# Performance work log

Measured on AMD Instinct MI355X. Metric: run time of the kernel, lower is better.

The kernel has to match this reference:

```python
import jax, jax.numpy as jnp
import numpy as np

KSIZE, STRIDE, H, W = 7, 4, 128, 128
NH = (H - KSIZE) // STRIDE + 1  # 31
L = NH * NH                     # 961 patches


def conv2d(x, w, b=None, stride=1):
    y = jax.lax.conv_general_dilated(x, w, (stride, stride), 'VALID',
                                     dimension_numbers=('NCHW', 'OIHW', 'NCHW'))
    if b is not None:
        y = y + b[None, :, None, None]
    return y


def refpad(x):
    return jnp.pad(x, ((0, 0), (0, 0), (1, 1), (1, 1)), mode='reflect')


def unfold(x, k, s):
    # torch.nn.Unfold equivalent, returned as (B, C, k, k, L)
    B, C, Hh, Ww = x.shape
    nh = (Hh - k) // s + 1
    nw = (Ww - k) // s + 1
    hi = (jnp.arange(nh) * s)[:, None] + jnp.arange(k)  # (nh, k)
    wi = (jnp.arange(nw) * s)[:, None] + jnp.arange(k)  # (nw, k)
    p = x[:, :, hi]            # (B, C, nh, k, W)
    p = p[:, :, :, :, wi]      # (B, C, nh, k, nw, k)
    p = p.transpose(0, 1, 3, 5, 2, 4).reshape(B, C, k, k, nh * nw)
    return p


def fold(patches, Hh, Ww, k, s):
    # patches: (B, nh, nw, C, k, k); overlap-add like torch.nn.functional.fold
    B, nh, nw, C = patches.shape[0], patches.shape[1], patches.shape[2], patches.shape[3]
    hi = (jnp.arange(nh) * s)[:, None] + jnp.arange(k)  # (nh, k)
    wi = (jnp.arange(nw) * s)[:, None] + jnp.arange(k)  # (nw, k)
    H_idx = hi[:, None, :, None]  # (nh, 1, k, 1)
    W_idx = wi[None, :, None, :]  # (1, nw, 1, k)
    vals = patches.transpose(0, 3, 1, 2, 4, 5)  # (B, C, nh, nw, k, k)
    out = jnp.zeros((B, C, Hh, Ww), patches.dtype)
    return out.at[:, :, H_idx, W_idx].add(vals)


def setup_inputs() -> dict:
    key = jax.random.key(0)
    ks = jax.random.split(key, 16)
    Cin, Ci = 32, 16            # in_channels, inter_channels
    F_in = KSIZE * KSIZE * Ci   # 784
    F_out = F_in // 4           # 196
    s = 0.05
    d = {
        'x':       jax.random.normal(ks[0], (8, Cin, H, W), jnp.float32),
        'g_w':     jax.random.normal(ks[1], (Ci, Cin, 3, 3), jnp.float32) * s,
        'g_b':     jax.random.normal(ks[2], (Ci,), jnp.float32) * s,
        'w_w':     jax.random.normal(ks[3], (Ci, Cin, 3, 3), jnp.float32) * s,
        'w_b':     jax.random.normal(ks[4], (Ci,), jnp.float32) * s,
        'theta_w': jax.random.normal(ks[5], (Cin, Ci, 1, 1), jnp.float32) * s,
        'theta_b': jax.random.normal(ks[6], (Cin,), jnp.float32) * s,
        'fc1_w':   jax.random.normal(ks[7], (F_out, F_in), jnp.float32) * s,
        'fc1_b':   jax.random.normal(ks[8], (F_out,), jnp.float32) * s,
        'mconv_w': jax.random.normal(ks[9], (L, L), jnp.float32) * s,
        'mconv_b': jax.random.normal(ks[10], (L,), jnp.float32) * s,
        'mfc_w':   jax.random.normal(ks[11], (L, L), jnp.float32) * s,
        'mfc_b':   jax.random.normal(ks[12], (L,), jnp.float32) * s,
        'c1_w':    jax.random.normal(ks[13], (Cin // 2, Cin, 3, 3), jnp.float32) * s,
        'c2_w':    jax.random.normal(ks[14], (Cin, Cin // 2, 1, 1), jnp.float32) * s,
    }
    return d


def reference(x, g_w, g_b, w_w, w_b, theta_w, theta_b, fc1_w, fc1_b,
              mconv_w, mconv_b, mfc_w, mfc_b, c1_w, c2_w):
    residual = x
    x1 = conv2d(refpad(x), g_w, g_b)        # (B, Ci, H, W)
    x2 = conv2d(refpad(x), w_w, w_b)        # (B, Ci, H, W)
    x3 = conv2d(x1, theta_w, theta_b)       # (B, Cin, H, W)
    B = x.shape[0]
    Cin = x.shape[1]

    p6 = unfold(x1, KSIZE, STRIDE).transpose(0, 4, 1, 2, 3).reshape(B, L, -1)   # (B,L,Ci*49)
    p4 = unfold(x2, KSIZE, STRIDE).transpose(0, 4, 1, 2, 3).reshape(B, L, -1)   # (B,L,Ci*49)
    p62 = unfold(x3, KSIZE, STRIDE).transpose(0, 4, 1, 2, 3).reshape(B, L, -1)  # (B,L,Cin*49)

    wf = p4 @ fc1_w.T + fc1_b   # (B, L, F)
    xf = p6 @ fc1_w.T + fc1_b   # (B, L, F)
    A = jnp.einsum('blf,bmf->blm', wf, xf)  # (B, L, L)

    # Ti1 (Conv1d k=1 over patch dim) + Ti2 (Linear over patch dim, transposed)
    Ti = jnp.einsum('nc,bcm->bnm', mconv_w + mfc_w, A) + (mconv_b + mfc_b)[None, :, None]
    mask = jax.nn.sigmoid(Ti)
    mask_b = (mask != 0.0).astype(A.dtype)

    scale = wf.shape[-1] ** -0.5
    Am = jax.nn.softmax(A * mask * scale, axis=-1) * mask_b  # (B, L, L)

    y = jnp.einsum('blm,bmf->blf', Am, p62)  # (B, L, Cin*49)
    y = y.reshape(B, NH, NH, Cin, KSIZE, KSIZE)
    out = fold(y, H, W, KSIZE, STRIDE)       # (B, Cin, H, W)

    # BasicBlock: conv3x3(reflect) -> lrelu -> conv1x1 -> lrelu
    o = jax.nn.leaky_relu(conv2d(refpad(out), c1_w), 0.2)
    o = jax.nn.leaky_relu(conv2d(o, c2_w), 0.2)
    out = residual + o
    return Am, out
```

## Files before the change

### kernel.cpp

```cpp
#include <hip/hip_runtime.h>
#include <math.h>

namespace {
constexpr int Bn   = 8;
constexpr int CIN  = 32;
constexpr int CI   = 16;
constexpr int Lp   = 961;
constexpr int FIN  = 784;
constexpr int FOUT = 196;
constexpr int F62  = 1568;

constexpr int FCP  = 224;
constexpr long long FCB = 961LL * FCP;
constexpr int KP   = 992;
constexpr long long WFTB = 196LL * KP;
constexpr long long AMBB = 961LL * KP;
constexpr long long PBTB = 1568LL * KP;
constexpr long long AB   = 961LL * 961;
constexpr int YLD  = 964;
constexpr long long YB = 1568LL * YLD;
}

typedef __attribute__((ext_vector_type(8))) short short8x;
typedef __attribute__((ext_vector_type(4))) float floatx4;
typedef __attribute__((ext_vector_type(4))) unsigned short ushort4x;

static __device__ __forceinline__ unsigned short f2bf(float x) {
    unsigned int u = __builtin_bit_cast(unsigned int, x);
    u += 0x7fffu + ((u >> 16) & 1u);
    return (unsigned short)(u >> 16);
}
static __device__ __forceinline__ float bf2f(unsigned short h) {
    return __builtin_bit_cast(float, ((unsigned int)h) << 16);
}

__global__ __launch_bounds__(256)
void prep_k(const float* __restrict__ g_w, const float* __restrict__ w_w,
            const float* __restrict__ c1_w,
            float* __restrict__ wT1, float* __restrict__ wT2,
            float* __restrict__ wTc,
            const float* __restrict__ mconv_w, const float* __restrict__ mfc_w,
            unsigned short* __restrict__ Mwh, unsigned short* __restrict__ Mwl,
            const float* __restrict__ mconv_b, const float* __restrict__ mfc_b,
            float* __restrict__ Mb,
            const float* __restrict__ fc1w,
            unsigned short* __restrict__ Wh, unsigned short* __restrict__ Wl,
            unsigned short* __restrict__ wfTh, unsigned short* __restrict__ wfTl)
{
    int i = blockIdx.x * 256 + threadIdx.x;
    if (i < 13824) {
        int sel = i / 4608, r = i - sel * 4608;
        int tapidx = r >> 4, co = r & 15;
        const float* w = (sel == 0) ? g_w : (sel == 1) ? w_w : c1_w;
        float* t = (sel == 0) ? wT1 : (sel == 1) ? wT2 : wTc;
        t[r] = w[co * 288 + tapidx];
    } else if (i < 967136) {
        int k = i - 13824;
        int n = k / KP, c = k - n * KP;
        float v = (c < 961) ? (mconv_w[n * 961 + c] + mfc_w[n * 961 + c]) : 0.0f;
        unsigned short h = f2bf(v);
        Mwh[k] = h; Mwl[k] = f2bf(v - bf2f(h));
    } else if (i < 968097) {
        int k = i - 967136;
        Mb[k] = mconv_b[k] + mfc_b[k];
    } else if (i < 1172897) {
        int k = i - 968097;
        int n = k / 800, kk = k - n * 800;
        float v = (n < 196 && kk < 784) ? fc1w[n * 784 + kk] : 0.0f;
        unsigned short h = f2bf(v);
        Wh[k] = h; Wl[k] = f2bf(v - bf2f(h));
    } else if (i < 1223073) {
        int k = i - 1172897;
        int row = k >> 5, c = k & 31;
        long long pos = (long long)row * KP + 960 + c;
        wfTh[pos] = 0; wfTl[pos] = 0;
    }
}

template<bool DUAL, bool BIAS, bool LEAKY>
__global__ __launch_bounds__(256)
void conv3x3t_k(const float* __restrict__ x,
                const float* __restrict__ wT1, const float* __restrict__ b1,
                const float* __restrict__ wT2, const float* __restrict__ b2,
                float* __restrict__ o1, float* __restrict__ o2)
{
    __shared__ float Ls[10880];
    const int tid = threadIdx.x;
    const int t  = blockIdx.x;
    const int wt = t & 3, ht = (t >> 2) & 15, b = t >> 6;
    const int h0 = ht * 8, w0 = wt * 32;
    const float* xb = x + (size_t)b * CIN * 16384;

    for (int i = tid; i < 10880; i += 256) {
        int ci  = i / 340;
        int rem = i - ci * 340;
        int row = rem / 34;
        int col = rem - row * 34;
        int gh = h0 + row - 1; gh = (gh < 0) ? 1 : (gh > 127 ? 126 : gh);
        int gw = w0 + col - 1; gw = (gw < 0) ? 1 : (gw > 127 ? 126 : gw);
        Ls[i] = xb[ci * 16384 + gh * 128 + gw];
    }
    __syncthreads();

    const int px = tid & 31, py = tid >> 5;
    float acc1[16], acc2[16];
    #pragma unroll
    for (int co = 0; co < 16; ++co) {
        acc1[co] = BIAS ? b1[co] : 0.0f;
        acc2[co] = (DUAL && BIAS) ? b2[co] : 0.0f;
    }

    for (int ci = 0; ci < 32; ++ci) {
        const float* lp = &Ls[ci * 340 + py * 34 + px];
        float vv[9];
        #pragma unroll
        for (int r = 0; r < 3; ++r)
            #pragma unroll
            for (int c = 0; c < 3; ++c)
                vv[r * 3 + c] = lp[r * 34 + c];
        const float* wr1 = wT1 + ci * 144;
        const float* wr2 = DUAL ? (wT2 + ci * 144) : nullptr;
        #pragma unroll
        for (int tp = 0; tp < 9; ++tp) {
            float v = vv[tp];
            #pragma unroll
            for (int co = 0; co < 16; ++co) {
                acc1[co] += v * wr1[tp * 16 + co];
                if constexpr (DUAL) acc2[co] += v * wr2[tp * 16 + co];
            }
        }
    }

    const int h = h0 + py, w = w0 + px;
    size_t ob = (((size_t)b * 16) * 128 + h) * 128 + w;
    #pragma unroll
    for (int co = 0; co < 16; ++co) {
        float v = acc1[co];
        if constexpr (LEAKY) v = (v >= 0.0f) ? v : 0.2f * v;
        o1[ob + (size_t)co * 16384] = v;
        if constexpr (DUAL) o2[ob + (size_t)co * 16384] = acc2[co];
    }
}

template<bool BIAS, bool LEAKY, bool RESID>
__global__ __launch_bounds__(256)
void conv1x1p_k(const float* __restrict__ src, const float* __restrict__ wgt,
                const float* __restrict__ bias, const float* __restrict__ resid,
                float* __restrict__ out)
{
    int idx = blockIdx.x * 256 + threadIdx.x;
    int pix = idx & 16383;
    int b   = idx >> 14;
    const float* sb = src + (size_t)b * CI * 16384 + pix;
    float s[16];
    #pragma unroll
    for (int ci = 0; ci < CI; ++ci) s[ci] = sb[ci * 16384];
    size_t ob = (size_t)b * 32 * 16384 + pix;
    #pragma unroll
    for (int co = 0; co < 32; ++co) {
        const float* wrow = wgt + co * CI;
        float acc = BIAS ? bias[co] : 0.0f;
        #pragma unroll
        for (int ci = 0; ci < CI; ++ci) acc += wrow[ci] * s[ci];
        if constexpr (LEAKY) acc = (acc >= 0.0f) ? acc : 0.2f * acc;
        if constexpr (RESID) acc += resid[ob + (size_t)co * 16384];
        out[ob + (size_t)co * 16384] = acc;
    }
}

template<bool WRT>
__global__ __launch_bounds__(256)
void fcmfma_k(const float* __restrict__ xsrc,
              const unsigned short* __restrict__ Wh,
              const unsigned short* __restrict__ Wl,
              const float* __restrict__ bias,
              unsigned short* __restrict__ Dh, unsigned short* __restrict__ Dl,
              unsigned short* __restrict__ DTh, unsigned short* __restrict__ DTl)
{
    __shared__ unsigned short AsH[64*32], AsL[64*32], BsH[64*32], BsL[64*32];
    const int tid = threadIdx.x;
    const int tm0 = (blockIdx.x >> 2) * 64;
    const int tn0 = (blockIdx.x & 3) * 64;

    const int lr = tid >> 2;
    const int lc = tid & 3;
    const int gm = tm0 + lr;
    const bool mok = gm < 7688;
    int gbase = 0;
    if (mok) {
        int b = gm / 961, pi = gm - b * 961;
        int ih = pi / 31, iw = pi - ih * 31;
        gbase = b * 262144 + ih * 512 + iw * 4;
    }
    const int pc = ((lc ^ ((lr >> 1) & 3))) * 8;
    const unsigned short* Whr = Wh + (tn0 + lr) * 800;
    const unsigned short* Wlr = Wl + (tn0 + lr) * 800;

    const int lane = tid & 63, wv = tid >> 6;
    const int wm = (wv >> 1) * 32, wn = (wv & 1) * 32;
    const int fr = lane & 15, kq = lane >> 4;

    floatx4 acc[2][2];
    #pragma unroll
    for (int i = 0; i < 2; ++i)
        #pragma unroll
        for (int j = 0; j < 2; ++j)
            acc[i][j] = (floatx4){0.f, 0.f, 0.f, 0.f};

    float pv[8];
    short8x pwh, pwl;
    auto loadA = [&](int k0) {
        #pragma unroll
        for (int j = 0; j < 8; ++j) {
            int k = k0 + lc * 8 + j;
            float v = 0.0f;
            if (mok && k < 784) {
                int c  = k / 49, r = k - c * 49;
                int kh = r / 7,  kw = r - kh * 7;
                v = xsrc[gbase + c * 16384 + kh * 128 + kw];
            }
            pv[j] = v;
        }
    };
    auto loadW = [&](int k0) {
        pwh = *(const short8x*)(Whr + k0 + lc * 8);
        pwl = *(const short8x*)(Wlr + k0 + lc * 8);
    };

    loadA(0); loadW(0);
    for (int k0 = 0; k0 < 800; k0 += 32) {
        unsigned short hv[8], lv[8];
        #pragma unroll
        for (int j = 0; j < 8; ++j) {
            unsigned short h = f2bf(pv[j]);
            hv[j] = h; lv[j] = f2bf(pv[j] - bf2f(h));
        }
        *(short8x*)&AsH[lr * 32 + pc] = *(short8x*)hv;
        *(short8x*)&AsL[lr * 32 + pc] = *(short8x*)lv;
        *(short8x*)&BsH[lr * 32 + pc] = pwh;
        *(short8x*)&BsL[lr * 32 + pc] = pwl;
        __syncthreads();
        if (k0 + 32 < 800) { loadA(k0 + 32); loadW(k0 + 32); }
        short8x ah[2], al[2], bh[2], bl[2];
        #pragma unroll
        for (int i = 0; i < 2; ++i) {
            int mr = wm + i * 16 + fr;
            int off = mr * 32 + ((kq ^ ((mr >> 1) & 3)) * 8);
            ah[i] = *(const short8x*)&AsH[off];
            al[i] = *(const short8x*)&AsL[off];
        }
        #pragma unroll
        for (int j = 0; j < 2; ++j) {
            int nr = wn + j * 16 + fr;
            int off = nr * 32 + ((kq ^ ((nr >> 1) & 3)) * 8);
            bh[j] = *(const short8x*)&BsH[off];
            bl[j] = *(const short8x*)&BsL[off];
        }
        #pragma unroll
        for (int i = 0; i < 2; ++i)
            #pragma unroll
            for (int j = 0; j < 2; ++j) {
                acc[i][j] = __builtin_amdgcn_mfma_f32_16x16x32_bf16(ah[i], bh[j], acc[i][j], 0, 0, 0);
                acc[i][j] = __builtin_amdgcn_mfma_f32_16x16x32_bf16(ah[i], bl[j], acc[i][j], 0, 0, 0);
                acc[i][j] = __builtin_amdgcn_mfma_f32_16x16x32_bf16(al[i], bh[j], acc[i][j], 0, 0, 0);
            }
        __syncthreads();
    }

    #pragma unroll
    for (int j = 0; j < 2; ++j) {
        int n = tn0 + wn + j * 16 + fr;
        if (n >= FCP) continue;
        float bn = (n < 196) ? bias[n] : 0.0f;
        #pragma unroll
        for (int i = 0; i < 2; ++i) {
            #pragma unroll
            for (int r = 0; r < 4; ++r) {
                int l = tm0 + wm + i * 16 + kq * 4 + r;
                if (l >= 7688) continue;
                int b = l / 961, pi = l - b * 961;
                float v = (n < 196) ? (acc[i][j][r] + bn) : 0.0f;
                unsigned short h = f2bf(v);
                unsigned short lo = f2bf(v - bf2f(h));
                long long base = (long long)b * FCB + (long long)pi * FCP + n;
                Dh[base] = h;
                Dl[base] = lo;
                if constexpr (WRT) {
                    if (n < 196) {
                        long long tb = (long long)b * WFTB + (long long)n * KP + pi;
                        DTh[tb] = h;
                        DTl[tb] = lo;
                    }
                }
            }
        }
    }
}

__global__ __launch_bounds__(256)
void w2mfma_k(const unsigned short* __restrict__ Xhi,
              const unsigned short* __restrict__ Xlo,
              const unsigned short* __restrict__ Yhi,
              const unsigned short* __restrict__ Ylo,
              unsigned short* __restrict__ W2h,
              unsigned short* __restrict__ W2l)
{
    __shared__ unsigned short XsH[4096], XsL[4096], YsH[4096], YsL[4096];
    const int b   = blockIdx.x & 7;
    const int t   = blockIdx.x >> 3;
    const int tm0 = (t >> 1) * 128;
    const int tn0 = (t & 1) * 128;
    const unsigned short* Ybh = Yhi + (long long)b * WFTB;
    const unsigned short* Ybl = Ylo + (long long)b * WFTB;
    const int tid = threadIdx.x;

    const int sr  = tid >> 1;
    const int sc0 = (tid & 1) * 2;
    const bool xok = (tm0 + sr) < 961;
    const bool yok = (tn0 + sr) < 196;
    const unsigned short* Xrh = Xhi + (long long)(tm0 + sr) * KP;
    const unsigned short* Xrl = Xlo + (long long)(tm0 + sr) * KP;
    const unsigned short* Yrh = Ybh + (long long)(tn0 + sr) * KP;
    const unsigned short* Yrl = Ybl + (long long)(tn0 + sr) * KP;
    const int swz = (sr >> 1) & 3;

    const int lane = tid & 63;
    const int wv   = tid >> 6;
    const int wm   = (wv >> 1) * 64, wn = (wv & 1) * 64;
    const int fr   = lane & 15;
    const int kq   = lane >> 4;

    floatx4 acc[4][4];
    #pragma unroll
    for (int i = 0; i < 4; ++i)
        #pragma unroll
        for (int j = 0; j < 4; ++j)
            acc[i][j] = (floatx4){0.f, 0.f, 0.f, 0.f};

    const short8x zz = {0,0,0,0,0,0,0,0};
    short8x pxh[2], pxl[2], pyh[2], pyl[2];
    auto loadK = [&](int k0) {
        #pragma unroll
        for (int c = 0; c < 2; ++c) {
            int kc = sc0 + c;
            pxh[c] = xok ? *(const short8x*)(Xrh + k0 + kc * 8) : zz;
            pxl[c] = xok ? *(const short8x*)(Xrl + k0 + kc * 8) : zz;
            pyh[c] = yok ? *(const short8x*)(Yrh + k0 + kc * 8) : zz;
            pyl[c] = yok ? *(const short8x*)(Yrl + k0 + kc * 8) : zz;
        }
    };

    loadK(0);
    for (int k0 = 0; k0 < KP; k0 += 32) {
        #pragma unroll
        for (int c = 0; c < 2; ++c) {
            int pc = (sc0 + c) ^ swz;
            *(short8x*)&XsH[sr * 32 + pc * 8] = pxh[c];
            *(short8x*)&XsL[sr * 32 + pc * 8] = pxl[c];
            *(short8x*)&YsH[sr * 32 + pc * 8] = pyh[c];
            *(short8x*)&YsL[sr * 32 + pc * 8] = pyl[c];
        }
        __syncthreads();
        if (k0 + 32 < KP) loadK(k0 + 32);
        short8x bh[4], bl[4];
        #pragma unroll
        for (int j = 0; j < 4; ++j) {
            int nr = wn + j * 16 + fr;
            int off = nr * 32 + ((kq ^ ((nr >> 1) & 3)) * 8);
            bh[j] = *(const short8x*)&YsH[off];
            bl[j] = *(const short8x*)&YsL[off];
        }
        #pragma unroll
        for (int i = 0; i < 4; ++i) {
            int mr = wm + i * 16 + fr;
            int off = mr * 32 + ((kq ^ ((mr >> 1) & 3)) * 8);
            short8x ah = *(const short8x*)&XsH[off];
            short8x al = *(const short8x*)&XsL[off];
            #pragma unroll
            for (int j = 0; j < 4; ++j) {
                acc[i][j] = __builtin_amdgcn_mfma_f32_16x16x32_bf16(ah, bh[j], acc[i][j], 0, 0, 0);
                acc[i][j] = __builtin_amdgcn_mfma_f32_16x16x32_bf16(ah, bl[j], acc[i][j], 0, 0, 0);
                acc[i][j] = __builtin_amdgcn_mfma_f32_16x16x32_bf16(al, bh[j], acc[i][j], 0, 0, 0);
            }
        }
        __syncthreads();
    }

    unsigned short* Wh2 = W2h + (long long)b * FCB;
    unsigned short* Wl2 = W2l + (long long)b * FCB;
    #pragma unroll
    for (int j = 0; j < 4; ++j) {
        int f = tn0 + wn + j * 16 + fr;
        if (f >= FCP) continue;
        #pragma unroll
        for (int i = 0; i < 4; ++i) {
            int lb = tm0 + wm + i * 16 + kq * 4;
            #pragma unroll
            for (int r = 0; r < 4; ++r) {
                int l = lb + r;
                if (l >= 961) continue;
                float v = acc[i][j][r];
                unsigned short h = f2bf(v);
                long long pos = (long long)l * FCP + f;
                Wh2[pos] = h;
                Wl2[pos] = f2bf(v - bf2f(h));
            }
        }
    }
}

__global__ __launch_bounds__(256, 2)
void atimfma_k(const unsigned short* __restrict__ Wfh,
               const unsigned short* __restrict__ Wfl,
               const unsigned short* __restrict__ W2h,
               const unsigned short* __restrict__ W2l,
               const unsigned short* __restrict__ Xfh,
               const unsigned short* __restrict__ Xfl,
               const float* __restrict__ Mb,
               float* __restrict__ Sout)
{
    const int b   = blockIdx.x & 7;
    const int t   = blockIdx.x >> 3;
    const int tm0 = (t >> 3) * 128;
    const int tn0 = (t & 7) * 128;
    const int tid = threadIdx.x;

    const int lane = tid & 63;
    const int wv   = tid >> 6;
    const int wm   = (wv >> 1) * 64, wn = (wv & 1) * 64;
    const int fr   = lane & 15;
    const int kq   = lane >> 4;

    const long long bb = (long long)b * FCB;
    const unsigned short* A1h = Wfh + bb;
    const unsigned short* A1l = Wfl + bb;
    const unsigned short* A2h = W2h + bb;
    const unsigned short* A2l = W2l + bb;
    const unsigned short* Byh = Xfh + bb;
    const unsigned short* Byl = Xfl + bb;

    int aoff[4], boff[4];
    #pragma unroll
    for (int i = 0; i < 4; ++i) {
        int r = tm0 + wm + i * 16 + fr; if (r > 960) r = 960;
        aoff[i] = r * FCP + kq * 8;
    }
    #pragma unroll
    for (int j = 0; j < 4; ++j) {
        int r = tn0 + wn + j * 16 + fr; if (r > 960) r = 960;
        boff[j] = r * FCP + kq * 8;
    }

    floatx4 accA[4][4], accT[4][4];
    #pragma unroll
    for (int i = 0; i < 4; ++i)
        #pragma unroll
        for (int j = 0; j < 4; ++j) {
            accA[i][j] = (floatx4){0.f, 0.f, 0.f, 0.f};
            accT[i][j] = (floatx4){0.f, 0.f, 0.f, 0.f};
        }

    short8x f1h[2][4], f1l[2][4], f2h[2][4], f2l[2][4], fbh[2][4], fbl[2][4];

    #pragma unroll
    for (int j = 0; j < 4; ++j) {
        fbh[0][j] = *(const short8x*)(Byh + boff[j]);
        fbl[0][j] = *(const short8x*)(Byl + boff[j]);
    }
    #pragma unroll
    for (int i = 0; i < 4; ++i) {
        f1h[0][i] = *(const short8x*)(A1h + aoff[i]);
        f1l[0][i] = *(const short8x*)(A1l + aoff[i]);
        f2h[0][i] = *(const short8x*)(A2h + aoff[i]);
        f2l[0][i] = *(const short8x*)(A2l + aoff[i]);
    }

    #pragma unroll
    for (int ks = 0; ks < 7; ++ks) {
        const int cur = ks & 1, nxt = cur ^ 1;
        if (ks < 6) {
            const int k0 = (ks + 1) * 32;
            #pragma unroll
            for (int j = 0; j < 4; ++j) {
                fbh[nxt][j] = *(const short8x*)(Byh + boff[j] + k0);
                fbl[nxt][j] = *(const short8x*)(Byl + boff[j] + k0);
            }
            #pragma unroll
            for (int i = 0; i < 4; ++i) {
                f1h[nxt][i] = *(const short8x*)(A1h + aoff[i] + k0);
                f1l[nxt][i] = *(const short8x*)(A1l + aoff[i] + k0);
                f2h[nxt][i] = *(const short8x*)(A2h + aoff[i] + k0);
                f2l[nxt][i] = *(const short8x*)(A2l + aoff[i] + k0);
            }
        }
        #pragma unroll
        for (int i = 0; i < 4; ++i) {
            #pragma unroll
            for (int j = 0; j < 4; ++j) {
                accA[i][j] = __builtin_amdgcn_mfma_f32_16x16x32_bf16(f1h[cur][i], fbh[cur][j], accA[i][j], 0, 0, 0);
                accA[i][j] = __builtin_amdgcn_mfma_f32_16x16x32_bf16(f1h[cur][i], fbl[cur][j], accA[i][j], 0, 0, 0);
                accA[i][j] = __builtin_amdgcn_mfma_f32_16x16x32_bf16(f1l[cur][i], fbh[cur][j], accA[i][j], 0, 0, 0);
                accT[i][j] = __builtin_amdgcn_mfma_f32_16x16x32_bf16(f2h[cur][i], fbh[cur][j], accT[i][j], 0, 0, 0);
                accT[i][j] = __builtin_amdgcn_mfma_f32_16x16x32_bf16(f2h[cur][i], fbl[cur][j], accT[i][j], 0, 0, 0);
                accT[i][j] = __builtin_amdgcn_mfma_f32_16x16x32_bf16(f2l[cur][i], fbh[cur][j], accT[i][j], 0, 0, 0);
            }
        }
    }

    const float scale = 0.07142857142857142f;
    float* Sb = Sout + (long long)b * AB;
    #pragma unroll
    for (int j = 0; j < 4; ++j) {
        int m = tn0 + wn + j * 16 + fr;
        if (m >= 961) continue;
        #pragma unroll
        for (int i = 0; i < 4; ++i) {
            int lb = tm0 + wm + i * 16 + kq * 4;
            #pragma unroll
            for (int r = 0; r < 4; ++r) {
                int l = lb + r;
                if (l >= 961) continue;
                float ti = accT[i][j][r] + Mb[l];
                float mask = 1.0f / (1.0f + expf(-ti));
                Sb[(long long)l * 961 + m] = accA[i][j][r] * mask * scale;
            }
        }
    }
}

__global__ __launch_bounds__(256)
void softmax_mask_k(const float* __restrict__ S, float* __restrict__ Am,
                    unsigned short* __restrict__ Amb)
{
    int row = blockIdx.x;
    const float* srow = S + (long long)row * Lp;
    float*       orow = Am + (long long)row * Lp;
    unsigned short* brow = Amb + (long long)row * KP;
    int tid = threadIdx.x;

    float s[4], mb[4];
    float lmax = -INFINITY;
    #pragma unroll
    for (int j = 0; j < 4; ++j) {
        int m = tid + j * 256;
        if (m < Lp) {
            float v = srow[m];
            s[j]  = v;
            mb[j] = (v != 0.0f) ? 1.0f : 0.0f;
            lmax  = fmaxf(lmax, v);
        } else { s[j] = -INFINITY; mb[j] = 0.0f; }
    }
    __shared__ float red[256];
    red[tid] = lmax; __syncthreads();
    #pragma unroll
    for (int off = 128; off > 0; off >>= 1) {
        if (tid < off) red[tid] = fmaxf(red[tid], red[tid + off]);
        __syncthreads();
    }
    float rmax = red[0];
    __syncthreads();

    float e[4];
    float lsum = 0.0f;
    #pragma unroll
    for (int j = 0; j < 4; ++j) {
        int m = tid + j * 256;
        e[j] = (m < Lp) ? expf(s[j] - rmax) : 0.0f;
        lsum += e[j];
    }
    red[tid] = lsum; __syncthreads();
    #pragma unroll
    for (int off = 128; off > 0; off >>= 1) {
        if (tid < off) red[tid] += red[tid + off];
        __syncthreads();
    }
    float inv = 1.0f / red[0];
    #pragma unroll
    for (int j = 0; j < 4; ++j) {
        int m = tid + j * 256;
        if (m < Lp) {
            float v = e[j] * inv * mb[j];
            orow[m] = v;
            brow[m] = f2bf(v);
        } else if (m < KP) {
            brow[m] = 0;
        }
    }
}

__global__ __launch_bounds__(256)
void p62bt_k(const float* __restrict__ x3, unsigned short* __restrict__ out)
{
    int idx = blockIdx.x * 256 + threadIdx.x;
    if (idx >= 8 * 1568 * 124) return;
    int ck = idx % 124;
    int t  = idx / 124;
    int n  = t % 1568;
    int b  = t / 1568;
    int c = n / 49, rr = n - c * 49;
    int kh = rr / 7, kw = rr - kh * 7;
    const float* src = x3 + (long long)b * 524288 + c * 16384 + kh * 128 + kw;
    int k = ck * 8;
    unsigned short v[8];
    #pragma unroll
    for (int j = 0; j < 8; ++j) {
        int kk = k + j;
        if (kk < Lp) {
            int ih = kk / 31, iw = kk - ih * 31;
            v[j] = f2bf(src[ih * 512 + iw * 4]);
        } else v[j] = 0;
    }
    *(short8x*)(out + ((long long)b * 1568 + n) * KP + k) = *(short8x*)v;
}

__global__ __launch_bounds__(256)
void ymfma_k(const unsigned short* __restrict__ Amb,
             const unsigned short* __restrict__ Pbt,
             unsigned short* __restrict__ yT)
{
    __shared__ unsigned short As[128 * 32];
    __shared__ unsigned short Bs[128 * 32];
    const int b   = blockIdx.x & 7;
    const int t   = blockIdx.x >> 3;
    const int tn0 = (t % 13) * 128;
    const int tm0 = (t / 13) * 128;
    const unsigned short* Ab = Amb + (long long)b * AMBB;
    const unsigned short* Bb = Pbt + (long long)b * PBTB;
    const int tid = threadIdx.x;

    const int sr  = tid >> 1;
    const int sc0 = (tid & 1) * 2;
    const bool aok = (tm0 + sr) < Lp;
    const bool bok = (tn0 + sr) < F62;
    const unsigned short* Arow = Ab + (long long)(tm0 + sr) * KP;
    const unsigned short* Brow = Bb + (long long)(tn0 + sr) * KP;
    const int swz = (sr >> 1) & 3;

    const int lane = tid & 63;
    const int wv   = tid >> 6;
    const int wm   = (wv >> 1) * 64, wn = (wv & 1) * 64;
    const int fr   = lane & 15;
    const int kq   = lane >> 4;

    floatx4 acc[4][4];
    #pragma unroll
    for (int i = 0; i < 4; ++i)
        #pragma unroll
        for (int j = 0; j < 4; ++j)
            acc[i][j] = (floatx4){0.f, 0.f, 0.f, 0.f};

    const short8x zz = {0,0,0,0,0,0,0,0};
    short8x pa[2], pb[2];
    auto loadK = [&](int k0) {
        #pragma unroll
        for (int c = 0; c < 2; ++c) {
            int kc = sc0 + c;
            pa[c] = aok ? *(const short8x*)(Arow + k0 + kc * 8) : zz;
            pb[c] = bok ? *(const short8x*)(Brow + k0 + kc * 8) : zz;
        }
    };

    loadK(0);
    for (int k0 = 0; k0 < Lp; k0 += 32) {
        #pragma unroll
        for (int c = 0; c < 2; ++c) {
            int pc = (sc0 + c) ^ swz;
            *(short8x*)&As[sr * 32 + pc * 8] = pa[c];
            *(short8x*)&Bs[sr * 32 + pc * 8] = pb[c];
        }
        __syncthreads();
        if (k0 + 32 < Lp) loadK(k0 + 32);
        short8x af[4], bfr[4];
        #pragma unroll
        for (int i = 0; i < 4; ++i) {
            int mr = wm + i * 16 + fr;
            af[i] = *(const short8x*)&As[mr * 32 + ((kq ^ ((mr >> 1) & 3)) * 8)];
        }
        #pragma unroll
        for (int j = 0; j < 4; ++j) {
            int nr = wn + j * 16 + fr;
            bfr[j] = *(const short8x*)&Bs[nr * 32 + ((kq ^ ((nr >> 1) & 3)) * 8)];
        }
        #pragma unroll
        for (int i = 0; i < 4; ++i)
            #pragma unroll
            for (int j = 0; j < 4; ++j)
                acc[i][j] = __builtin_amdgcn_mfma_f32_16x16x32_bf16(
                                af[i], bfr[j], acc[i][j], 0, 0, 0);
        __syncthreads();
    }

    unsigned short* Yb = yT + (long long)b * YB;
    #pragma unroll
    for (int j = 0; j < 4; ++j) {
        int n = tn0 + wn + j * 16 + fr;
        if (n >= F62) continue;
        unsigned short* Yr = Yb + (long long)n * YLD;
        #pragma unroll
        for (int i = 0; i < 4; ++i) {
            int lb = tm0 + wm + i * 16 + kq * 4;
            if (lb >= Lp) continue;
            ushort4x hv;
            #pragma unroll
            for (int r = 0; r < 4; ++r) hv[r] = f2bf(acc[i][j][r]);
            if (lb + 3 < Lp) {
                *(ushort4x*)(Yr + lb) = hv;
            } else {
                #pragma unroll
                for (int r = 0; r < 4; ++r)
                    if (lb + r < Lp) Yr[lb + r] = hv[r];
            }
        }
    }
}

__global__ __launch_bounds__(256)
void foldg_k(const unsigned short* __restrict__ yT, float* __restrict__ out)
{
    int idx = blockIdx.x * 256 + threadIdx.x;
    int wc = idx & 127;
    int hr = (idx >> 7) & 127;
    int c  = (idx >> 14) & 31;
    int b  = idx >> 19;
    int ih_lo = (hr >= 6) ? ((hr - 3) >> 2) : 0;
    int ih_hi = min(hr >> 2, 30);
    int iw_lo = (wc >= 6) ? ((wc - 3) >> 2) : 0;
    int iw_hi = min(wc >> 2, 30);
    const unsigned short* Yb = yT + (long long)b * YB + (long long)c * 49 * YLD;
    float acc = 0.0f;
    for (int ih = ih_lo; ih <= ih_hi; ++ih) {
        int kh = hr - 4 * ih;
        for (int iw = iw_lo; iw <= iw_hi; ++iw) {
            int kw = wc - 4 * iw;
            acc += bf2f(Yb[(kh * 7 + kw) * YLD + ih * 31 + iw]);
        }
    }
    out[idx] = acc;
}

extern "C" void kernel_launch(void* const* d_in, const int* in_sizes, int n_in,
                              void* d_out, int out_size, void* d_ws, size_t ws_size,
                              hipStream_t stream)
{
    const float* x       = (const float*)d_in[0];
    const float* g_w     = (const float*)d_in[1];
    const float* g_b     = (const float*)d_in[2];
    const float* w_w     = (const float*)d_in[3];
    const float* w_b     = (const float*)d_in[4];
    const float* theta_w = (const float*)d_in[5];
    const float* theta_b = (const float*)d_in[6];
    const float* fc1_w   = (const float*)d_in[7];
    const float* fc1_b   = (const float*)d_in[8];
    const float* mconv_w = (const float*)d_in[9];
    const float* mconv_b = (const float*)d_in[10];
    const float* mfc_w   = (const float*)d_in[11];
    const float* mfc_b   = (const float*)d_in[12];
    const float* c1_w    = (const float*)d_in[13];
    const float* c2_w    = (const float*)d_in[14];

    float* Am_out    = (float*)d_out;
    float* final_out = Am_out + (size_t)Bn * Lp * Lp;

    float* ws = (float*)d_ws;
    float* x1    = ws;
    float* x2    = ws + 2097152;
    float* x3    = ws + 4194304;
    unsigned short* xf_hi = (unsigned short*)(ws + 8388608);
    unsigned short* xf_lo = (unsigned short*)(ws + 9249664);
    unsigned short* wf_hi = (unsigned short*)(ws + 10110720);
    unsigned short* wf_lo = (unsigned short*)(ws + 10971776);
    float* Abuf  = ws + 11832832;
    unsigned short* wfT_hi = (unsigned short*)(ws + 19221000);
    unsigned short* wfT_lo = (unsigned short*)(ws + 19998728);
    unsigned short* W2_hi  = (unsigned short*)(ws + 20776456);
    unsigned short* W2_lo  = (unsigned short*)(ws + 21637512);
    unsigned short* Mw_hi = (unsigned short*)(ws + 26847496);
    unsigned short* Mw_lo = (unsigned short*)(ws + 27324152);
    float* Mb    = ws + 27800808;
    unsigned short* fc1wh = (unsigned short*)(ws + 27801832);
    unsigned short* fc1wl = (unsigned short*)(ws + 27904232);
    float* wT1   = ws + 28006632;
    float* wT2   = ws + 28011240;
    float* wTc   = ws + 28015848;
    unsigned short* Am_bf16 = (unsigned short*)x1;
    unsigned short* p62bT   = (unsigned short*)Abuf;
    unsigned short* yT      = wfT_hi;

    prep_k<<<4778, 256, 0, stream>>>(
        g_w, w_w, c1_w, wT1, wT2, wTc,
        mconv_w, mfc_w, Mw_hi, Mw_lo,
        mconv_b, mfc_b, Mb, fc1_w, fc1wh, fc1wl,
        wfT_hi, wfT_lo);

    conv3x3t_k<true, true, false><<<512, 256, 0, stream>>>(
        x, wT1, g_b, wT2, w_b, x1, x2);

    conv1x1p_k<true, false, false><<<512, 256, 0, stream>>>(
        x1, theta_w, theta_b, nullptr, x3);

    fcmfma_k<false><<<484, 256, 0, stream>>>(
        x1, fc1wh, fc1wl, fc1_b, xf_hi, xf_lo, nullptr, nullptr);
    fcmfma_k<true><<<484, 256, 0, stream>>>(
        x2, fc1wh, fc1wl, fc1_b, wf_hi, wf_lo, wfT_hi, wfT_lo);

    w2mfma_k<<<128, 256, 0, stream>>>(
        Mw_hi, Mw_lo, wfT_hi, wfT_lo, W2_hi, W2_lo);

    atimfma_k<<<512, 256, 0, stream>>>(
        wf_hi, wf_lo, W2_hi, W2_lo, xf_hi, xf_lo, Mb, Abuf);

    softmax_mask_k<<<7688, 256, 0, stream>>>(Abuf, Am_out, Am_bf16);

    p62bt_k<<<6077, 256, 0, stream>>>(x3, p62bT);

    ymfma_k<<<832, 256, 0, stream>>>(Am_bf16, p62bT, yT);

    foldg_k<<<16384, 256, 0, stream>>>(yT, x3);

    conv3x3t_k<false, false, true><<<512, 256, 0, stream>>>(
        x3, wTc, nullptr, nullptr, nullptr, x1, nullptr);

    conv1x1p_k<false, true, true><<<512, 256, 0, stream>>>(
        x1, c2_w, nullptr, x, final_out);
}
```

Before: 525.8 us.

## Rewrite 3x3 convolutions as implicit-GEMM using split-bf16 MFMA

Replaces the scalar FP32 3x3 convolution kernels with an implicit-GEMM kernel. Each block handles one image row: it gathers the reflect-padded im2col values (taps padded from 9 to 16 per channel), splits them into bf16 hi/lo parts in swizzled LDS, and accumulates with three bf16 MFMAs per product to approximate FP32 accuracy. The prep kernel now writes the conv weights as padded hi/lo bf16 matrices. The intent is to move the conv FLOPs onto matrix cores, at the cost of wasted padded taps, three MFMAs per product and a small accuracy change from dropping the lo*lo term.

```diff
diff --git a/kernel.cpp b/kernel.cpp
--- a/kernel.cpp
+++ b/kernel.cpp
@@ -19,6 +19,7 @@
 constexpr long long AB   = 961LL * 961;
 constexpr int YLD  = 964;
 constexpr long long YB = 1568LL * YLD;
+constexpr int CKP  = 512;
 }
 
 typedef __attribute__((ext_vector_type(8))) short short8x;
@@ -37,8 +38,8 @@
 __global__ __launch_bounds__(256)
 void prep_k(const float* __restrict__ g_w, const float* __restrict__ w_w,
             const float* __restrict__ c1_w,
-            float* __restrict__ wT1, float* __restrict__ wT2,
-            float* __restrict__ wTc,
+            unsigned short* __restrict__ cwh, unsigned short* __restrict__ cwl,
+            unsigned short* __restrict__ c1h, unsigned short* __restrict__ c1l,
             const float* __restrict__ mconv_w, const float* __restrict__ mfc_w,
             unsigned short* __restrict__ Mwh, unsigned short* __restrict__ Mwl,
             const float* __restrict__ mconv_b, const float* __restrict__ mfc_b,
@@ -48,97 +49,180 @@
             unsigned short* __restrict__ wfTh, unsigned short* __restrict__ wfTl)
 {
     int i = blockIdx.x * 256 + threadIdx.x;
-    if (i < 13824) {
-        int sel = i / 4608, r = i - sel * 4608;
-        int tapidx = r >> 4, co = r & 15;
-        const float* w = (sel == 0) ? g_w : (sel == 1) ? w_w : c1_w;
-        float* t = (sel == 0) ? wT1 : (sel == 1) ? wT2 : wTc;
-        t[r] = w[co * 288 + tapidx];
-    } else if (i < 967136) {
-        int k = i - 13824;
+    if (i < 16384) {
+        int n = i >> 9, k = i & 511;
+        int ci = k >> 4, t = k & 15;
+        float v = 0.0f;
+        if (t < 9) v = (n < 16) ? g_w[n * 288 + ci * 9 + t]
+                                : w_w[(n - 16) * 288 + ci * 9 + t];
+        unsigned short h = f2bf(v);
+        cwh[i] = h; cwl[i] = f2bf(v - bf2f(h));
+    } else if (i < 24576) {
+        int k2 = i - 16384;
+        int n = k2 >> 9, k = k2 & 511;
+        int ci = k >> 4, t = k & 15;
+        float v = (t < 9) ? c1_w[n * 288 + ci * 9 + t] : 0.0f;
+        unsigned short h = f2bf(v);
+        c1h[k2] = h; c1l[k2] = f2bf(v - bf2f(h));
+    } else if (i < 977888) {
+        int k = i - 24576;
         int n = k / KP, c = k - n * KP;
         float v = (c < 961) ? (mconv_w[n * 961 + c] + mfc_w[n * 961 + c]) : 0.0f;
         unsigned short h = f2bf(v);
         Mwh[k] = h; Mwl[k] = f2bf(v - bf2f(h));
-    } else if (i < 968097) {
-        int k = i - 967136;
+    } else if (i < 978849) {
+        int k = i - 977888;
         Mb[k] = mconv_b[k] + mfc_b[k];
-    } else if (i < 1172897) {
-        int k = i - 968097;
+    } else if (i < 1183649) {
+        int k = i - 978849;
         int n = k / 800, kk = k - n * 800;
         float v = (n < 196 && kk < 784) ? fc1w[n * 784 + kk] : 0.0f;
         unsigned short h = f2bf(v);
         Wh[k] = h; Wl[k] = f2bf(v - bf2f(h));
-    } else if (i < 1223073) {
-        int k = i - 1172897;
+    } else if (i < 1233825) {
+        int k = i - 1183649;
         int row = k >> 5, c = k & 31;
         long long pos = (long long)row * KP + 960 + c;
         wfTh[pos] = 0; wfTl[pos] = 0;
     }
 }
 
-template<bool DUAL, bool BIAS, bool LEAKY>
+template<int NOUT, bool BIAS, bool LEAKY>
 __global__ __launch_bounds__(256)
-void conv3x3t_k(const float* __restrict__ x,
-                const float* __restrict__ wT1, const float* __restrict__ b1,
-                const float* __restrict__ wT2, const float* __restrict__ b2,
+void convmfma_k(const float* __restrict__ x,
+                const unsigned short* __restrict__ Bh,
+                const unsigned short* __restrict__ Bl,
+                const float* __restrict__ b1, const float* __restrict__ b2,
                 float* __restrict__ o1, float* __restrict__ o2)
 {
-    __shared__ float Ls[10880];
+    __shared__ unsigned short AsH[128 * 32], AsL[128 * 32];
+    __shared__ unsigned short BsH[NOUT * 32], BsL[NOUT * 32];
+
     const int tid = threadIdx.x;
-    const int t  = blockIdx.x;
-    const int wt = t & 3, ht = (t >> 2) & 15, b = t >> 6;
-    const int h0 = ht * 8, w0 = wt * 32;
+    const int b   = blockIdx.x & 7;
+    const int h   = blockIdx.x >> 3;
     const float* xb = x + (size_t)b * CIN * 16384;
 
-    for (int i = tid; i < 10880; i += 256) {
-        int ci  = i / 340;
-        int rem = i - ci * 340;
-        int row = rem / 34;
-        int col = rem - row * 34;
-        int gh = h0 + row - 1; gh = (gh < 0) ? 1 : (gh > 127 ? 126 : gh);
-        int gw = w0 + col - 1; gw = (gw < 0) ? 1 : (gw > 127 ? 126 : gw);
-        Ls[i] = xb[ci * 16384 + gh * 128 + gw];
-    }
-    __syncthreads();
-
-    const int px = tid & 31, py = tid >> 5;
-    float acc1[16], acc2[16];
-    #pragma unroll
-    for (int co = 0; co < 16; ++co) {
-        acc1[co] = BIAS ? b1[co] : 0.0f;
-        acc2[co] = (DUAL && BIAS) ? b2[co] : 0.0f;
-    }
-
-    for (int ci = 0; ci < 32; ++ci) {
-        const float* lp = &Ls[ci * 340 + py * 34 + px];
-        float vv[9];
-        #pragma unroll
-        for (int r = 0; r < 3; ++r)
-            #pragma unroll
-            for (int c = 0; c < 3; ++c)
-                vv[r * 3 + c] = lp[r * 34 + c];
-        const float* wr1 = wT1 + ci * 144;
-        const float* wr2 = DUAL ? (wT2 + ci * 144) : nullptr;
-        #pragma unroll
-        for (int tp = 0; tp < 9; ++tp) {
-            float v = vv[tp];
-            #pragma unroll
-            for (int co = 0; co < 16; ++co) {
-                acc1[co] += v * wr1[tp * 16 + co];
-                if constexpr (DUAL) acc2[co] += v * wr2[tp * 16 + co];
-            }
-        }
-    }
-
-    const int h = h0 + py, w = w0 + px;
-    size_t ob = (((size_t)b * 16) * 128 + h) * 128 + w;
-    #pragma unroll
-    for (int co = 0; co < 16; ++co) {
-        float v = acc1[co];
-        if constexpr (LEAKY) v = (v >= 0.0f) ? v : 0.2f * v;
-        o1[ob + (size_t)co * 16384] = v;
-        if constexpr (DUAL) o2[ob + (size_t)co * 16384] = acc2[co];
+    const int m   = tid & 127;
+    const int kh2 = tid >> 7;
+    int ghr[3], gwc[3];
+    #pragma unroll
+    for (int r = 0; r < 3; ++r) {
+        int gh = h - 1 + r; ghr[r] = (gh < 0) ? 1 : (gh > 127 ? 126 : gh);
+        int gw = m - 1 + r; gwc[r] = (gw < 0) ? 1 : (gw > 127 ? 126 : gw);
+    }
+
+    const int lane = tid & 63;
+    const int wv   = tid >> 6;
+    const int wm   = wv * 32;
+    const int fr   = lane & 15;
+    const int kq   = lane >> 4;
+    constexpr int NF = NOUT / 16;
+
+    floatx4 acc[2][NF];
+    #pragma unroll
+    for (int i = 0; i < 2; ++i)
+        #pragma unroll
+        for (int j = 0; j < NF; ++j)
+            acc[i][j] = (floatx4){0.f, 0.f, 0.f, 0.f};
+
+    float pv[9];
+    short8x pbh0, pbh1, pbl0, pbl1;
+    const bool bstage = tid < NOUT * 2;
+    const int bn  = tid >> 1;
+    const int bk  = tid & 1;
+
+    auto loadA = [&](int ks) {
+        const float* src = xb + (ks * 2 + kh2) * 16384;
+        #pragma unroll
+        for (int j = 0; j < 9; ++j)
+            pv[j] = src[ghr[j / 3] * 128 + gwc[j % 3]];
+    };
+    auto loadB = [&](int ks) {
+        if (bstage) {
+            const unsigned short* sh = Bh + bn * CKP + ks * 32 + bk * 16;
+            const unsigned short* sl = Bl + bn * CKP + ks * 32 + bk * 16;
+            pbh0 = *(const short8x*)sh;       pbh1 = *(const short8x*)(sh + 8);
+            pbl0 = *(const short8x*)sl;       pbl1 = *(const short8x*)(sl + 8);
+        }
+    };
+
+    loadA(0); loadB(0);
+    for (int ks = 0; ks < 16; ++ks) {
+        {
+            unsigned short hv[16], lv[16];
+            #pragma unroll
+            for (int j = 0; j < 16; ++j) {
+                float v = (j < 9) ? pv[j] : 0.0f;
+                unsigned short hh = f2bf(v);
+                hv[j] = hh; lv[j] = f2bf(v - bf2f(hh));
+            }
+            const int swz = (m >> 1) & 3;
+            const int o0 = (kh2 * 2) ^ swz, o1o = (kh2 * 2 + 1) ^ swz;
+            *(short8x*)&AsH[m * 32 + o0 * 8]  = ((short8x*)hv)[0];
+            *(short8x*)&AsH[m * 32 + o1o * 8] = ((short8x*)hv)[1];
+            *(short8x*)&AsL[m * 32 + o0 * 8]  = ((short8x*)lv)[0];
+            *(short8x*)&AsL[m * 32 + o1o * 8] = ((short8x*)lv)[1];
+        }
+        if (bstage) {
+            const int swz = (bn >> 1) & 3;
+            const int o0 = (bk * 2) ^ swz, o1o = (bk * 2 + 1) ^ swz;
+            *(short8x*)&BsH[bn * 32 + o0 * 8]  = pbh0;
+            *(short8x*)&BsH[bn * 32 + o1o * 8] = pbh1;
+            *(short8x*)&BsL[bn * 32 + o0 * 8]  = pbl0;
+            *(short8x*)&BsL[bn * 32 + o1o * 8] = pbl1;
+        }
+        __syncthreads();
+        if (ks < 15) { loadA(ks + 1); loadB(ks + 1); }
+
+        short8x bhf[NF], blf[NF];
+        #pragma unroll
+        for (int j = 0; j < NF; ++j) {
+            int nr = j * 16 + fr;
+            int off = nr * 32 + ((kq ^ ((nr >> 1) & 3)) * 8);
+            bhf[j] = *(const short8x*)&BsH[off];
+            blf[j] = *(const short8x*)&BsL[off];
+        }
+        #pragma unroll
+        for (int i = 0; i < 2; ++i) {
+            int mr = wm + i * 16 + fr;
+            int off = mr * 32 + ((kq ^ ((mr >> 1) & 3)) * 8);
+            short8x ah = *(const short8x*)&AsH[off];
+            short8x al = *(const short8x*)&AsL[off];
+            #pragma unroll
+            for (int j = 0; j < NF; ++j) {
+                acc[i][j] = __builtin_amdgcn_mfma_f32_16x16x32_bf16(ah, bhf[j], acc[i][j], 0, 0, 0);
+                acc[i][j] = __builtin_amdgcn_mfma_f32_16x16x32_bf16(ah, blf[j], acc[i][j], 0, 0, 0);
+                acc[i][j] = __builtin_amdgcn_mfma_f32_16x16x32_bf16(al, bhf[j], acc[i][j], 0, 0, 0);
+            }
+        }
+        __syncthreads();
+    }
+
+    #pragma unroll
+    for (int j = 0; j < NF; ++j) {
+        int n = j * 16 + fr;
+        float bnv = 0.0f;
+        if constexpr (BIAS) bnv = (n < 16) ? b1[n] : b2[n - 16];
+        float* dst;
+        if constexpr (NOUT == 32) {
+            dst = (n < 16) ? (o1 + (((size_t)b * 16 + n) * 128 + h) * 128)
+                           : (o2 + (((size_t)b * 16 + (n - 16)) * 128 + h) * 128);
+        } else {
+            dst = o1 + (((size_t)b * 16 + n) * 128 + h) * 128;
+        }
+        #pragma unroll
+        for (int i = 0; i < 2; ++i) {
+            int wb = wm + i * 16 + kq * 4;
+            floatx4 ov;
+            #pragma unroll
+            for (int r = 0; r < 4; ++r) {
+                float v = acc[i][j][r] + bnv;
+                if constexpr (LEAKY) v = (v >= 0.0f) ? v : 0.2f * v;
+                ov[r] = v;
+            }
+            *(floatx4*)(dst + wb) = ov;
+        }
     }
 }
 
@@ -779,21 +863,22 @@
     float* Mb    = ws + 27800808;
     unsigned short* fc1wh = (unsigned short*)(ws + 27801832);
     unsigned short* fc1wl = (unsigned short*)(ws + 27904232);
-    float* wT1   = ws + 28006632;
-    float* wT2   = ws + 28011240;
-    float* wTc   = ws + 28015848;
+    unsigned short* cwh = (unsigned short*)(ws + 4194304);
+    unsigned short* cwl = cwh + 16384;
+    unsigned short* c1h = (unsigned short*)(ws + 28006632);
+    unsigned short* c1l = c1h + 8192;
     unsigned short* Am_bf16 = (unsigned short*)x1;
     unsigned short* p62bT   = (unsigned short*)Abuf;
     unsigned short* yT      = wfT_hi;
 
-    prep_k<<<4778, 256, 0, stream>>>(
-        g_w, w_w, c1_w, wT1, wT2, wTc,
+    prep_k<<<4821, 256, 0, stream>>>(
+        g_w, w_w, c1_w, cwh, cwl, c1h, c1l,
         mconv_w, mfc_w, Mw_hi, Mw_lo,
         mconv_b, mfc_b, Mb, fc1_w, fc1wh, fc1wl,
         wfT_hi, wfT_lo);
 
-    conv3x3t_k<true, true, false><<<512, 256, 0, stream>>>(
-        x, wT1, g_b, wT2, w_b, x1, x2);
+    convmfma_k<32, true, false><<<1024, 256, 0, stream>>>(
+        x, cwh, cwl, g_b, w_b, x1, x2);
 
     conv1x1p_k<true, false, false><<<512, 256, 0, stream>>>(
         x1, theta_w, theta_b, nullptr, x3);
@@ -817,8 +902,8 @@
 
     foldg_k<<<16384, 256, 0, stream>>>(yT, x3);
 
-    conv3x3t_k<false, false, true><<<512, 256, 0, stream>>>(
-        x3, wTc, nullptr, nullptr, nullptr, x1, nullptr);
+    convmfma_k<16, false, true><<<1024, 256, 0, stream>>>(
+        x3, c1h, c1l, nullptr, nullptr, x1, nullptr);
 
     conv1x1p_k<false, true, true><<<512, 256, 0, stream>>>(
         x1, c2_w, nullptr, x, final_out);
```

New measurement: 476.6 us. -9.4%, faster.
